# Kernel optimization log

Hardware: AMD Instinct MI355X
Metric: run time of the kernel (lower is better)

The kernel has to match this reference:

```python
import jax, jax.numpy as jnp
import numpy as np

B, T, C, H = 16, 2048, 1024, 64

def setup_inputs() -> dict:
    key = jax.random.key(0)
    kx, kq, kk, kv = jax.random.split(key, 4)
    x = jax.random.normal(kx, (B, T, C), dtype=jnp.float32)
    Wq = jax.random.normal(kq, (C, H), dtype=jnp.float32) * (C ** -0.5)
    Wk = jax.random.normal(kk, (C, H), dtype=jnp.float32) * (C ** -0.5)
    Wv = jax.random.normal(kv, (C, H), dtype=jnp.float32) * (C ** -0.5)
    return {"x": x, "Wq": Wq, "Wk": Wk, "Wv": Wv}

def reference(x, Wq, Wk, Wv):
    # q,k,v: [B,T,H]
    q = jnp.einsum('btc,ch->bth', x, Wq)
    k = jnp.einsum('btc,ch->bth', x, Wk)
    v = jnp.einsum('btc,ch->bth', x, Wv)
    scale = k.shape[-1] ** -0.5
    # scores: [B,T,T], causal mask then softmax (dropout=0 -> identity)
    w = jnp.einsum('bth,bsh->bts', q, k) * scale
    causal = jnp.tril(jnp.ones((x.shape[1], x.shape[1]), dtype=bool))
    w = jnp.where(causal[None, :, :], w, -jnp.inf)
    w = jax.nn.softmax(w, axis=-1)
    out = jnp.einsum('bts,bsh->bth', w, v)
    return out
```

## Files before the change

### kernel.cpp

```cpp
#include <hip/hip_runtime.h>


#define B_ 16
#define T_ 2048
#define C_ 1024
#define H_ 64
#define QK_ELEMS (B_ * T_ * H_)

typedef float  f32x4  __attribute__((ext_vector_type(4)));
typedef __bf16 bf16x8 __attribute__((ext_vector_type(8)));
typedef __bf16 bf16x4 __attribute__((ext_vector_type(4)));

__device__ __forceinline__ void glds16(const void* g, void* l) {
    __builtin_amdgcn_global_load_lds(
        (const __attribute__((address_space(1))) void*)g,
        (__attribute__((address_space(3))) void*)l, 16, 0, 0);
}

__global__ __launch_bounds__(256) void wt_kernel(const float* __restrict__ Wq,
                                                 const float* __restrict__ Wk,
                                                 const float* __restrict__ Wv,
                                                 __bf16* __restrict__ Wt) {
    __shared__ float tl[64][65];
    const int mat = blockIdx.x >> 4;
    const int c0  = (blockIdx.x & 15) * 64;
    const float* W = (mat == 0) ? Wq : (mat == 1) ? Wk : Wv;
    const int t  = threadIdx.x;
    const int r4 = t >> 6;
    const int cc = t & 63;
#pragma unroll
    for (int i = 0; i < 16; i++) {
        const int c = r4 + i * 4;
        tl[c][cc] = W[(size_t)(c0 + c) * H_ + cc];
    }
    __syncthreads();
#pragma unroll
    for (int i = 0; i < 16; i++) {
        const int h = r4 + i * 4;
        const int cc2 = ((((cc >> 3) ^ (h & 7)) << 3) | (cc & 7));
        Wt[(size_t)mat * 65536 + (size_t)h * C_ + c0 + cc2] = (__bf16)tl[cc][h];
    }
}

__global__ __launch_bounds__(256) void qkv_kernel(const float* __restrict__ x,
                                                  const __bf16* __restrict__ Wt,
                                                  __bf16* __restrict__ Qw,
                                                  __bf16* __restrict__ Kw,
                                                  __bf16* __restrict__ Vtw) {
    __shared__ __align__(16) __bf16 Alds[2][64 * 72];
    __shared__ __align__(16) __bf16 Blds[2][192 * 64];

    const int tid  = threadIdx.x;
    const int w    = tid >> 6;
    const int lane = tid & 63;
    const int quad = lane >> 4;
    const int l15  = lane & 15;
    const int wm   = (w & 1) * 32;
    const int wn   = (w >> 1) * 96;
    const int m0   = blockIdx.x * 64;

    f32x4 acc[12];
#pragma unroll
    for (int i = 0; i < 12; i++) acc[i] = (f32x4){0.f, 0.f, 0.f, 0.f};

    const int ar = tid >> 3;
    const int ac = (tid & 7) * 8;
    const float* xA = x + (size_t)(m0 + ar) * C_ + ac;
    const __bf16* bsrc = Wt + (size_t)(w * 48 + (lane >> 3)) * C_ + (lane & 7) * 8;

    float4 a[2][4];
    auto loadA = [&](int slot, int k0) {
        a[slot][0] = *(const float4*)(xA + k0);
        a[slot][1] = *(const float4*)(xA + k0 + 4);
        a[slot][2] = *(const float4*)(xA + k0 + 32 * C_);
        a[slot][3] = *(const float4*)(xA + k0 + 32 * C_ + 4);
    };
    auto storeA = [&](int slot, int buf) {
        bf16x8 v0, v1;
        v0[0]=(__bf16)a[slot][0].x; v0[1]=(__bf16)a[slot][0].y;
        v0[2]=(__bf16)a[slot][0].z; v0[3]=(__bf16)a[slot][0].w;
        v0[4]=(__bf16)a[slot][1].x; v0[5]=(__bf16)a[slot][1].y;
        v0[6]=(__bf16)a[slot][1].z; v0[7]=(__bf16)a[slot][1].w;
        v1[0]=(__bf16)a[slot][2].x; v1[1]=(__bf16)a[slot][2].y;
        v1[2]=(__bf16)a[slot][2].z; v1[3]=(__bf16)a[slot][2].w;
        v1[4]=(__bf16)a[slot][3].x; v1[5]=(__bf16)a[slot][3].y;
        v1[6]=(__bf16)a[slot][3].z; v1[7]=(__bf16)a[slot][3].w;
        *(bf16x8*)&Alds[buf][ar * 72 + ac]        = v0;
        *(bf16x8*)&Alds[buf][(ar + 32) * 72 + ac] = v1;
    };
    auto asyncB = [&](int k0, int buf) {
        __bf16* dst = &Blds[buf][(w * 48) * 64];
        const __bf16* src = bsrc + k0;
#pragma unroll
        for (int i = 0; i < 6; i++)
            glds16(src + (size_t)i * 8 * C_, dst + i * 8 * 64);
    };

    loadA(0, 0); loadA(1, 64);
    asyncB(0, 0);
    storeA(0, 0);

    for (int k = 0; k < 16; k++) {
        __syncthreads();
        const int kn = k + 1;
        if (kn < 16) asyncB(kn * 64, kn & 1);
        if (k + 2 < 16) loadA(k & 1, (k + 2) * 64);
        const int buf = k & 1;
#pragma unroll
        for (int kh = 0; kh < 2; kh++) {
            bf16x8 af0 = *(const bf16x8*)&Alds[buf][(wm + l15) * 72 + kh * 32 + quad * 8];
            bf16x8 af1 = *(const bf16x8*)&Alds[buf][(wm + 16 + l15) * 72 + kh * 32 + quad * 8];
            const int ch8 = ((((kh << 2) + quad) ^ (l15 & 7)) << 3);
#pragma unroll
            for (int nt = 0; nt < 6; nt++) {
                bf16x8 bfr = *(const bf16x8*)&Blds[buf][(wn + nt * 16 + l15) * 64 + ch8];
                acc[nt]     = __builtin_amdgcn_mfma_f32_16x16x32_bf16(af0, bfr, acc[nt], 0, 0, 0);
                acc[6 + nt] = __builtin_amdgcn_mfma_f32_16x16x32_bf16(af1, bfr, acc[6 + nt], 0, 0, 0);
            }
        }
        if (kn < 16) storeA(kn & 1, kn & 1);
    }

#pragma unroll
    for (int mt = 0; mt < 2; mt++) {
        const int row0 = m0 + wm + mt * 16 + quad * 4;
#pragma unroll
        for (int nt = 0; nt < 6; nt++) {
            const int col = wn + nt * 16 + l15;
            const f32x4 acv = acc[mt * 6 + nt];
            if (wn + nt * 16 < 64) {
#pragma unroll
                for (int r = 0; r < 4; r++)
                    Qw[(size_t)(row0 + r) * H_ + col] = (__bf16)acv[r];
            } else if (wn + nt * 16 < 128) {
                const int h = col - 64;
#pragma unroll
                for (int r = 0; r < 4; r++) {
                    const int row = row0 + r;
                    const int hs  = (((h >> 3) ^ (row & 7)) << 3) | (h & 7);
                    Kw[(size_t)row * H_ + hs] = (__bf16)acv[r];
                }
            }
        }
    }
    __bf16* Vt_l = &Alds[0][0];
    if (w >= 2) {
#pragma unroll
        for (int mt = 0; mt < 2; mt++) {
            const int t0 = wm + mt * 16 + quad * 4;
#pragma unroll
            for (int nt = 2; nt < 6; nt++) {
                const int h = (nt - 2) * 16 + l15;
                const f32x4 acv = acc[mt * 6 + nt];
                bf16x4 pv;
                pv[0]=(__bf16)acv[0]; pv[1]=(__bf16)acv[1];
                pv[2]=(__bf16)acv[2]; pv[3]=(__bf16)acv[3];
                *(bf16x4*)&Vt_l[h * 72 + t0] = pv;
            }
        }
    }
    __syncthreads();
    if (w >= 2) {
        const int bb   = m0 >> 11;
        const int tblk = m0 & 2047;
#pragma unroll
        for (int i = 0; i < 4; i++) {
            const int hh = (w - 2) * 32 + i * 8 + (lane >> 3);
            const int cs = (((lane & 7) ^ (lane >> 3)) << 3);
            *(bf16x8*)(Vtw + (((size_t)(bb * H_ + hh)) << 11) + tblk + ((lane & 7) << 3)) =
                *(const bf16x8*)&Vt_l[hh * 72 + cs];
        }
    }
}

#define SCALE_LOG2E 0.18033688011112042f

__global__ __launch_bounds__(256) void attn_kernel(const __bf16* __restrict__ Qw,
                                                   const __bf16* __restrict__ Kw,
                                                   const __bf16* __restrict__ Vtw,
                                                   float* __restrict__ Opart,
                                                   float* __restrict__ Lpart) {
    __shared__ __align__(16) __bf16 Klds[2][64 * 64];
    __shared__ __align__(16) __bf16 Vlds[2][64 * 64];
    __shared__ __align__(16) __bf16 Plds[2][4][16 * 72];

    const int tid  = threadIdx.x;
    const int w    = tid >> 6;
    const int lane = tid & 63;
    const int quad = lane >> 4;
    const int l15  = lane & 15;

    const int b   = blockIdx.x & 15;
    const int cid = blockIdx.x >> 4;
    int i, ci;
    if (cid < 16)      { i = 15 - (cid >> 2); ci = cid & 3; }
    else if (cid < 28) { const int u = cid - 16; i = 11 - u / 3; ci = u % 3; }
    else if (cid < 36) { const int u = cid - 28; i = 7 - (u >> 1); ci = u & 1; }
    else               { i = 3 - (cid - 36); ci = 0; }

    const int jmax = 2 * i + 1;
    const int j0 = ci * 8;
    const int j1 = (j0 + 8 < jmax + 1) ? j0 + 8 : jmax + 1;
    const int nj = j1 - j0;
    const int qA0 = 2 * i * 64;
    const size_t bT = (size_t)b * T_;

    const __bf16* qpA = Qw + (bT + qA0 + w * 16 + l15) * H_ + quad * 8;
    const bf16x8 qfA0 = *(const bf16x8*)qpA;
    const bf16x8 qfA1 = *(const bf16x8*)(qpA + 32);
    const bf16x8 qfB0 = *(const bf16x8*)(qpA + 64 * H_);
    const bf16x8 qfB1 = *(const bf16x8*)(qpA + 64 * H_ + 32);

    float lA = 0.f, lB = 0.f;
    f32x4 accA[4], accB[4];
#pragma unroll
    for (int nt = 0; nt < 4; nt++) {
        accA[nt] = (f32x4){0.f, 0.f, 0.f, 0.f};
        accB[nt] = (f32x4){0.f, 0.f, 0.f, 0.f};
    }

    auto stage = [&](int ts0, int buf) {
        const __bf16* Ks = Kw + (bT + ts0) * H_;
        const __bf16* Vs = Vtw + (((size_t)(b * H_)) << 11) + ts0;
#pragma unroll
        for (int c = 0; c < 2; c++) {
            const int g   = w * 2 + c;
            const int row = g * 8 + (lane >> 3);
            const int cb  = (lane & 7) * 8;
            glds16(Ks + (size_t)row * H_ + cb, &Klds[buf][g * 512]);
            glds16(Vs + ((size_t)row << 11) + cb, &Vlds[buf][g * 512]);
        }
    };

    stage(j0 * 64, 0);

    for (int jj = 0; jj < nj; jj++) {
        const int j = j0 + jj;
        __syncthreads();
        if (jj + 1 < nj) stage((j + 1) * 64, (jj + 1) & 1);
        const int buf = jj & 1;
        const bool doA = (j <= 2 * i);
        const int ts0 = j * 64;
        const int qgA = qA0 + w * 16 + l15;

#pragma unroll
        for (int nt = 0; nt < 4; nt++) {
            const __bf16* kb = &Klds[buf][(nt * 16 + l15) * 64];
            bf16x8 kf0 = *(const bf16x8*)(kb + ((quad ^ (l15 & 7)) << 3));
            bf16x8 kf1 = *(const bf16x8*)(kb + (((4 + quad) ^ (l15 & 7)) << 3));
            const int key0 = ts0 + nt * 16 + quad * 4;

            if (doA) {
                f32x4 z = (f32x4){0.f, 0.f, 0.f, 0.f};
                z = __builtin_amdgcn_mfma_f32_16x16x32_bf16(kf0, qfA0, z, 0, 0, 0);
                z = __builtin_amdgcn_mfma_f32_16x16x32_bf16(kf1, qfA1, z, 0, 0, 0);
                bf16x4 pv;
#pragma unroll
                for (int r = 0; r < 4; r++) {
                    float e = exp2f(__builtin_fmaf(z[r], SCALE_LOG2E, -8.0f));
                    if (j == 2 * i && key0 + r > qgA) e = 0.f;
                    pv[r] = (__bf16)e;
                    lA += e;
                }
                *(bf16x4*)&Plds[0][w][l15 * 72 + nt * 16 + quad * 4] = pv;
            }
            {
                f32x4 z = (f32x4){0.f, 0.f, 0.f, 0.f};
                z = __builtin_amdgcn_mfma_f32_16x16x32_bf16(kf0, qfB0, z, 0, 0, 0);
                z = __builtin_amdgcn_mfma_f32_16x16x32_bf16(kf1, qfB1, z, 0, 0, 0);
                bf16x4 pv;
#pragma unroll
                for (int r = 0; r < 4; r++) {
                    float e = exp2f(__builtin_fmaf(z[r], SCALE_LOG2E, -8.0f));
                    if (j == jmax && key0 + r > qgA + 64) e = 0.f;
                    pv[r] = (__bf16)e;
                    lB += e;
                }
                *(bf16x4*)&Plds[1][w][l15 * 72 + nt * 16 + quad * 4] = pv;
            }
        }
        __asm__ __volatile__("s_waitcnt lgkmcnt(0)" ::: "memory");

        const __bf16* prA = &Plds[0][w][l15 * 72];
        const __bf16* prB = &Plds[1][w][l15 * 72];
        bf16x8 pfA0, pfA1;
        if (doA) {
            pfA0 = *(const bf16x8*)(prA + quad * 8);
            pfA1 = *(const bf16x8*)(prA + 32 + quad * 8);
        }
        bf16x8 pfB0 = *(const bf16x8*)(prB + quad * 8);
        bf16x8 pfB1 = *(const bf16x8*)(prB + 32 + quad * 8);
#pragma unroll
        for (int nt = 0; nt < 4; nt++) {
            const __bf16* vb = &Vlds[buf][(nt * 16 + l15) * 64];
            bf16x8 vf0 = *(const bf16x8*)(vb + ((quad ^ (l15 & 7)) << 3));
            bf16x8 vf1 = *(const bf16x8*)(vb + (((4 + quad) ^ (l15 & 7)) << 3));
            if (doA) {
                accA[nt] = __builtin_amdgcn_mfma_f32_16x16x32_bf16(pfA0, vf0, accA[nt], 0, 0, 0);
                accA[nt] = __builtin_amdgcn_mfma_f32_16x16x32_bf16(pfA1, vf1, accA[nt], 0, 0, 0);
            }
            accB[nt] = __builtin_amdgcn_mfma_f32_16x16x32_bf16(pfB0, vf0, accB[nt], 0, 0, 0);
            accB[nt] = __builtin_amdgcn_mfma_f32_16x16x32_bf16(pfB1, vf1, accB[nt], 0, 0, 0);
        }
    }

    lA += __shfl_xor(lA, 16); lA += __shfl_xor(lA, 32);
    lB += __shfl_xor(lB, 16); lB += __shfl_xor(lB, 32);

    const int qiA = 2 * i;
    const int slotA = ((((b << 5) + qiA) << 2) + ci);
    const int slotB = ((((b << 5) + qiA + 1) << 2) + ci);
    float* OpA = Opart + (size_t)slotA * 4096;
    float* OpB = Opart + (size_t)slotB * 4096;
#pragma unroll
    for (int nt = 0; nt < 4; nt++)
#pragma unroll
        for (int r = 0; r < 4; r++) {
            const int o = (w * 16 + quad * 4 + r) * 64 + nt * 16 + l15;
            OpA[o] = accA[nt][r];
            OpB[o] = accB[nt][r];
        }
    if (quad == 0) {
        Lpart[slotA * 64 + w * 16 + l15] = lA;
        Lpart[slotB * 64 + w * 16 + l15] = lB;
    }
}

__global__ __launch_bounds__(256) void reduce_kernel(const float* __restrict__ Opart,
                                                     const float* __restrict__ Lpart,
                                                     float* __restrict__ out) {
    const int b  = blockIdx.x & 15;
    const int qi = blockIdx.x >> 4;
    const int nc = ((qi & ~1) + 9) >> 3;
    const int tid = threadIdx.x;
    const int q  = tid >> 2;
    const int hc = (tid & 3) * 16;
    const int sbase = ((b << 5) + qi) << 2;

    f32x4 s[4];
#pragma unroll
    for (int i = 0; i < 4; i++) s[i] = (f32x4){0.f, 0.f, 0.f, 0.f};
    float l = 0.f;
    for (int ci = 0; ci < nc; ci++) {
        const float* Op = Opart + (size_t)(sbase + ci) * 4096 + q * 64 + hc;
#pragma unroll
        for (int i = 0; i < 4; i++) s[i] += *(const f32x4*)(Op + i * 4);
        l += Lpart[(sbase + ci) * 64 + q];
    }
    const float inv = 1.f / l;
    float* o = out + ((size_t)b * T_ + qi * 64 + q) * H_ + hc;
#pragma unroll
    for (int i = 0; i < 4; i++) {
        f32x4 r = s[i] * inv;
        *(f32x4*)(o + i * 4) = r;
    }
}

extern "C" void kernel_launch(void* const* d_in, const int* in_sizes, int n_in,
                              void* d_out, int out_size, void* d_ws, size_t ws_size,
                              hipStream_t stream) {
    const float* x  = (const float*)d_in[0];
    const float* Wq = (const float*)d_in[1];
    const float* Wk = (const float*)d_in[2];
    const float* Wv = (const float*)d_in[3];
    float* out = (float*)d_out;

    __bf16* Qw  = (__bf16*)d_ws;
    __bf16* Kw  = Qw + QK_ELEMS;
    __bf16* Vtw = Kw + QK_ELEMS;
    __bf16* Wt  = Vtw + QK_ELEMS;
    float* Opart = (float*)((char*)d_ws + 16777216);
    float* Lpart = Opart + (size_t)2048 * 4096;

    wt_kernel<<<dim3(48), dim3(256), 0, stream>>>(Wq, Wk, Wv, Wt);
    qkv_kernel<<<dim3((B_ * T_) / 64), dim3(256), 0, stream>>>(x, Wt, Qw, Kw, Vtw);
    attn_kernel<<<dim3(640), dim3(256), 0, stream>>>(Qw, Kw, Vtw, Opart, Lpart);
    reduce_kernel<<<dim3(512), dim3(256), 0, stream>>>(Opart, Lpart, out);
}
```

Measured before the change: 242.6 us.

## Feed QKV projection MFMAs directly from global memory with register prefetch

The QKV projection kernel no longer stages x and W tiles through double-buffered LDS with async global-to-LDS copies and barriers. Each wave now loads its MFMA fragments straight from global memory into registers, with a three-deep software prefetch, and computes a 64x48 output slab. Each wave redundantly reads the whole 64-row x tile, which relies on cache hits to avoid extra global traffic. The weight transpose drops its LDS swizzle to match, and an occupancy hint of 2 blocks per CU is added.

```diff
diff --git a/kernel.cpp b/kernel.cpp
--- a/kernel.cpp
+++ b/kernel.cpp
@@ -37,138 +37,112 @@
 #pragma unroll
     for (int i = 0; i < 16; i++) {
         const int h = r4 + i * 4;
-        const int cc2 = ((((cc >> 3) ^ (h & 7)) << 3) | (cc & 7));
-        Wt[(size_t)mat * 65536 + (size_t)h * C_ + c0 + cc2] = (__bf16)tl[cc][h];
-    }
-}
-
-__global__ __launch_bounds__(256) void qkv_kernel(const float* __restrict__ x,
-                                                  const __bf16* __restrict__ Wt,
-                                                  __bf16* __restrict__ Qw,
-                                                  __bf16* __restrict__ Kw,
-                                                  __bf16* __restrict__ Vtw) {
-    __shared__ __align__(16) __bf16 Alds[2][64 * 72];
-    __shared__ __align__(16) __bf16 Blds[2][192 * 64];
+        Wt[(size_t)mat * 65536 + (size_t)h * C_ + c0 + cc] = (__bf16)tl[cc][h];
+    }
+}
+
+__global__ __launch_bounds__(256, 2) void qkv_kernel(const float* __restrict__ x,
+                                                     const __bf16* __restrict__ Wt,
+                                                     __bf16* __restrict__ Qw,
+                                                     __bf16* __restrict__ Kw,
+                                                     __bf16* __restrict__ Vtw) {
+    __shared__ __align__(16) __bf16 Vt_l[64 * 72];
 
     const int tid  = threadIdx.x;
     const int w    = tid >> 6;
     const int lane = tid & 63;
     const int quad = lane >> 4;
     const int l15  = lane & 15;
-    const int wm   = (w & 1) * 32;
-    const int wn   = (w >> 1) * 96;
     const int m0   = blockIdx.x * 64;
 
     f32x4 acc[12];
 #pragma unroll
     for (int i = 0; i < 12; i++) acc[i] = (f32x4){0.f, 0.f, 0.f, 0.f};
 
-    const int ar = tid >> 3;
-    const int ac = (tid & 7) * 8;
-    const float* xA = x + (size_t)(m0 + ar) * C_ + ac;
-    const __bf16* bsrc = Wt + (size_t)(w * 48 + (lane >> 3)) * C_ + (lane & 7) * 8;
-
-    float4 a[2][4];
-    auto loadA = [&](int slot, int k0) {
-        a[slot][0] = *(const float4*)(xA + k0);
-        a[slot][1] = *(const float4*)(xA + k0 + 4);
-        a[slot][2] = *(const float4*)(xA + k0 + 32 * C_);
-        a[slot][3] = *(const float4*)(xA + k0 + 32 * C_ + 4);
+    const float*  xb = x  + (size_t)(m0 + l15) * C_ + quad * 8;
+    const __bf16* wb = Wt + (size_t)(w * 48 + l15) * C_ + quad * 8;
+
+    float4 Aset[3][8];
+    bf16x8 Bset[3][3];
+
+    auto loadSet = [&](int h, int s) {
+#pragma unroll
+        for (int mt = 0; mt < 4; mt++) {
+            const float* p = xb + (size_t)mt * 16 * C_ + h * 32;
+            Aset[s][mt * 2]     = *(const float4*)p;
+            Aset[s][mt * 2 + 1] = *(const float4*)(p + 4);
+        }
+#pragma unroll
+        for (int nt = 0; nt < 3; nt++)
+            Bset[s][nt] = *(const bf16x8*)(wb + (size_t)nt * 16 * C_ + h * 32);
     };
-    auto storeA = [&](int slot, int buf) {
-        bf16x8 v0, v1;
-        v0[0]=(__bf16)a[slot][0].x; v0[1]=(__bf16)a[slot][0].y;
-        v0[2]=(__bf16)a[slot][0].z; v0[3]=(__bf16)a[slot][0].w;
-        v0[4]=(__bf16)a[slot][1].x; v0[5]=(__bf16)a[slot][1].y;
-        v0[6]=(__bf16)a[slot][1].z; v0[7]=(__bf16)a[slot][1].w;
-        v1[0]=(__bf16)a[slot][2].x; v1[1]=(__bf16)a[slot][2].y;
-        v1[2]=(__bf16)a[slot][2].z; v1[3]=(__bf16)a[slot][2].w;
-        v1[4]=(__bf16)a[slot][3].x; v1[5]=(__bf16)a[slot][3].y;
-        v1[6]=(__bf16)a[slot][3].z; v1[7]=(__bf16)a[slot][3].w;
-        *(bf16x8*)&Alds[buf][ar * 72 + ac]        = v0;
-        *(bf16x8*)&Alds[buf][(ar + 32) * 72 + ac] = v1;
-    };
-    auto asyncB = [&](int k0, int buf) {
-        __bf16* dst = &Blds[buf][(w * 48) * 64];
-        const __bf16* src = bsrc + k0;
-#pragma unroll
-        for (int i = 0; i < 6; i++)
-            glds16(src + (size_t)i * 8 * C_, dst + i * 8 * 64);
-    };
-
-    loadA(0, 0); loadA(1, 64);
-    asyncB(0, 0);
-    storeA(0, 0);
-
-    for (int k = 0; k < 16; k++) {
-        __syncthreads();
-        const int kn = k + 1;
-        if (kn < 16) asyncB(kn * 64, kn & 1);
-        if (k + 2 < 16) loadA(k & 1, (k + 2) * 64);
-        const int buf = k & 1;
-#pragma unroll
-        for (int kh = 0; kh < 2; kh++) {
-            bf16x8 af0 = *(const bf16x8*)&Alds[buf][(wm + l15) * 72 + kh * 32 + quad * 8];
-            bf16x8 af1 = *(const bf16x8*)&Alds[buf][(wm + 16 + l15) * 72 + kh * 32 + quad * 8];
-            const int ch8 = ((((kh << 2) + quad) ^ (l15 & 7)) << 3);
-#pragma unroll
-            for (int nt = 0; nt < 6; nt++) {
-                bf16x8 bfr = *(const bf16x8*)&Blds[buf][(wn + nt * 16 + l15) * 64 + ch8];
-                acc[nt]     = __builtin_amdgcn_mfma_f32_16x16x32_bf16(af0, bfr, acc[nt], 0, 0, 0);
-                acc[6 + nt] = __builtin_amdgcn_mfma_f32_16x16x32_bf16(af1, bfr, acc[6 + nt], 0, 0, 0);
-            }
-        }
-        if (kn < 16) storeA(kn & 1, kn & 1);
-    }
-
-#pragma unroll
-    for (int mt = 0; mt < 2; mt++) {
-        const int row0 = m0 + wm + mt * 16 + quad * 4;
-#pragma unroll
-        for (int nt = 0; nt < 6; nt++) {
-            const int col = wn + nt * 16 + l15;
-            const f32x4 acv = acc[mt * 6 + nt];
-            if (wn + nt * 16 < 64) {
+
+    loadSet(0, 0);
+    loadSet(1, 1);
+
+#pragma unroll
+    for (int h = 0; h < 32; h++) {
+        if (h + 2 < 32) loadSet(h + 2, (h + 2) % 3);
+        const int s = h % 3;
+        bf16x8 af[4];
+#pragma unroll
+        for (int mt = 0; mt < 4; mt++) {
+            const float4 f0 = Aset[s][mt * 2];
+            const float4 f1 = Aset[s][mt * 2 + 1];
+            af[mt][0] = (__bf16)f0.x; af[mt][1] = (__bf16)f0.y;
+            af[mt][2] = (__bf16)f0.z; af[mt][3] = (__bf16)f0.w;
+            af[mt][4] = (__bf16)f1.x; af[mt][5] = (__bf16)f1.y;
+            af[mt][6] = (__bf16)f1.z; af[mt][7] = (__bf16)f1.w;
+        }
+#pragma unroll
+        for (int mt = 0; mt < 4; mt++)
+#pragma unroll
+            for (int nt = 0; nt < 3; nt++)
+                acc[mt * 3 + nt] = __builtin_amdgcn_mfma_f32_16x16x32_bf16(
+                    af[mt], Bset[s][nt], acc[mt * 3 + nt], 0, 0, 0);
+    }
+
+#pragma unroll
+    for (int mt = 0; mt < 4; mt++) {
+        const int row0 = m0 + mt * 16 + quad * 4;
+#pragma unroll
+        for (int nt = 0; nt < 3; nt++) {
+            const int col = w * 48 + nt * 16 + l15;
+            const f32x4 a = acc[mt * 3 + nt];
+            if (col < 64) {
 #pragma unroll
                 for (int r = 0; r < 4; r++)
-                    Qw[(size_t)(row0 + r) * H_ + col] = (__bf16)acv[r];
-            } else if (wn + nt * 16 < 128) {
+                    Qw[(size_t)(row0 + r) * H_ + col] = (__bf16)a[r];
+            } else if (col < 128) {
                 const int h = col - 64;
 #pragma unroll
                 for (int r = 0; r < 4; r++) {
                     const int row = row0 + r;
                     const int hs  = (((h >> 3) ^ (row & 7)) << 3) | (h & 7);
-                    Kw[(size_t)row * H_ + hs] = (__bf16)acv[r];
+                    Kw[(size_t)row * H_ + hs] = (__bf16)a[r];
                 }
-            }
-        }
-    }
-    __bf16* Vt_l = &Alds[0][0];
-    if (w >= 2) {
-#pragma unroll
-        for (int mt = 0; mt < 2; mt++) {
-            const int t0 = wm + mt * 16 + quad * 4;
-#pragma unroll
-            for (int nt = 2; nt < 6; nt++) {
-                const int h = (nt - 2) * 16 + l15;
-                const f32x4 acv = acc[mt * 6 + nt];
+            } else {
+                const int h  = col - 128;
+                const int t0 = mt * 16 + quad * 4;
                 bf16x4 pv;
-                pv[0]=(__bf16)acv[0]; pv[1]=(__bf16)acv[1];
-                pv[2]=(__bf16)acv[2]; pv[3]=(__bf16)acv[3];
+                pv[0] = (__bf16)a[0]; pv[1] = (__bf16)a[1];
+                pv[2] = (__bf16)a[2]; pv[3] = (__bf16)a[3];
                 *(bf16x4*)&Vt_l[h * 72 + t0] = pv;
             }
         }
     }
     __syncthreads();
-    if (w >= 2) {
+    {
         const int bb   = m0 >> 11;
         const int tblk = m0 & 2047;
 #pragma unroll
-        for (int i = 0; i < 4; i++) {
-            const int hh = (w - 2) * 32 + i * 8 + (lane >> 3);
-            const int cs = (((lane & 7) ^ (lane >> 3)) << 3);
-            *(bf16x8*)(Vtw + (((size_t)(bb * H_ + hh)) << 11) + tblk + ((lane & 7) << 3)) =
-                *(const bf16x8*)&Vt_l[hh * 72 + cs];
+        for (int i = 0; i < 2; i++) {
+            const int idx = tid + i * 256;
+            const int h   = idx >> 3;
+            const int c   = idx & 7;
+            const int sc  = c ^ (h & 7);
+            *(bf16x8*)(Vtw + (((size_t)(bb * H_ + h)) << 11) + tblk + c * 8) =
+                *(const bf16x8*)&Vt_l[h * 72 + sc * 8];
         }
     }
 }
```

Result: slower. 291.2 us (+20.0%).
